# Kernel tuning notes

Measured on AMD Instinct MI355X. Metric: run time of the kernel, lower is better.

## Reference

```python
import jax, jax.numpy as jnp
import numpy as np

# --- static config (matches init_kwargs) ---
B = 2; HI = 60; WI = 60; T = 4; WS = 8; SHIFT = 4
C = 256; NH = 8; HD = C // NH; HID = 1024
P = HI * WI; N = T * P
PAD = (WS - HI % WS) % WS           # 4 -> pad 60 -> 64
HP = HI + PAD; WP = WI + PAD
NWH = HP // WS; NWW = WP // WS
L = WS * WS                          # 64 tokens per window
SCALE = HD ** -0.5

# relative position index [L, L] (constant)
_c = np.stack(np.meshgrid(np.arange(WS), np.arange(WS), indexing='ij')).reshape(2, -1)
_r = (_c[:, :, None] - _c[:, None, :]).transpose(1, 2, 0) + WS - 1
REL_IDX = jnp.asarray(_r[..., 0] * (2 * WS - 1) + _r[..., 1])

# per-window key padding mask [nWin, L] (True = padded token)
_b = np.zeros((HP, WP), bool); _b[HI:, :] = True; _b[:, WI:] = True
WIN_MASK = jnp.asarray(_b.reshape(NWH, WS, NWW, WS).transpose(0, 2, 1, 3).reshape(NWH * NWW, L))


def _ln(x, w, b):
    m = x.mean(-1, keepdims=True)
    v = jnp.square(x - m).mean(-1, keepdims=True)
    return (x - m) * jax.lax.rsqrt(v + 1e-5) * w + b


def _partition(x4):  # [Bm, HP, WP, C] -> [Bm*nWin, L, C]
    Bm = x4.shape[0]
    return x4.reshape(Bm, NWH, WS, NWW, WS, C).transpose(0, 1, 3, 2, 4, 5).reshape(Bm * NWH * NWW, L, C)


def _win_attn(xq, xkv, qw, qb, kw, kb, vw, vb, ow, ob, bias_table):
    Bm = B * T
    q4 = xq.reshape(Bm, HI, WI, C)
    k4 = xkv.reshape(Bm, HI, WI, C)
    q4 = jnp.roll(q4, (-SHIFT, -SHIFT), (1, 2))
    k4 = jnp.roll(k4, (-SHIFT, -SHIFT), (1, 2))
    pad = ((0, 0), (0, PAD), (0, PAD), (0, 0))
    q4 = jnp.pad(q4, pad); k4 = jnp.pad(k4, pad)
    q_win = _partition(q4)   # [Bw, L, C]
    kv_win = _partition(k4)
    q = (q_win @ qw.T + qb).reshape(-1, L, NH, HD)
    k = (kv_win @ kw.T + kb).reshape(-1, L, NH, HD)
    v = (kv_win @ vw.T + vb).reshape(-1, L, NH, HD)
    attn = jnp.einsum('bihd,bjhd->bhij', q, k) * SCALE
    attn = attn + bias_table[REL_IDX].transpose(2, 0, 1)[None]      # RPB [1,H,L,L]
    km = jnp.tile(WIN_MASK, (Bm, 1))                                  # [Bw, L]
    attn = jnp.where(km[:, None, None, :], -jnp.inf, attn)
    p = jax.nn.softmax(attn, axis=-1)
    o = jnp.einsum('bhij,bjhd->bihd', p, v).reshape(-1, L, C)
    o = o @ ow.T + ob
    y = o.reshape(Bm, NWH, NWW, WS, WS, C).transpose(0, 1, 3, 2, 4, 5).reshape(Bm, HP, WP, C)
    y = y[:, :HI, :WI, :]
    y = jnp.roll(y, (SHIFT, SHIFT), (1, 2))
    return y.reshape(B, N, C)


def reference(x, context, ln1_w, ln1_b, ln2_w, ln2_b, ln3_w, ln3_b, lnc_w, lnc_b,
              sa_q_w, sa_q_b, sa_k_w, sa_k_b, sa_v_w, sa_v_b, sa_o_w, sa_o_b, sa_bias,
              ca_q_w, ca_q_b, ca_k_w, ca_k_b, ca_v_w, ca_v_b, ca_o_w, ca_o_b, ca_bias,
              gamma1, gamma2, gamma_mlp, mlp_w1, mlp_b1, mlp_w2, mlp_b2):
    xn = _ln(x, ln1_w, ln1_b)
    y_s = _win_attn(xn, xn, sa_q_w, sa_q_b, sa_k_w, sa_k_b, sa_v_w, sa_v_b, sa_o_w, sa_o_b, sa_bias)
    x = x + gamma1 * y_s
    y_c = _win_attn(_ln(x, ln2_w, ln2_b), _ln(context, lnc_w, lnc_b),
                    ca_q_w, ca_q_b, ca_k_w, ca_k_b, ca_v_w, ca_v_b, ca_o_w, ca_o_b, ca_bias)
    x = x + gamma2 * y_c
    h = _ln(x, ln3_w, ln3_b)
    h = jax.nn.gelu(h @ mlp_w1.T + mlp_b1, approximate=False) @ mlp_w2.T + mlp_b2
    return x + gamma_mlp * h


def setup_inputs() -> dict:
    key = jax.random.key(0)
    ks = jax.random.split(key, 16)
    def w(k, shape, s=0.02):
        return jax.random.normal(k, shape, jnp.float32) * s
    inp = {}
    inp['x'] = jax.random.normal(ks[0], (B, N, C), jnp.float32)
    inp['context'] = jax.random.normal(ks[1], (B, N, C), jnp.float32)
    for nm in ['ln1', 'ln2', 'ln3', 'lnc']:
        inp[f'{nm}_w'] = jnp.ones((C,), jnp.float32)
        inp[f'{nm}_b'] = jnp.zeros((C,), jnp.float32)
    i = 2
    for pfx in ['sa', 'ca']:
        for pn in ['q', 'k', 'v', 'o']:
            inp[f'{pfx}_{pn}_w'] = w(ks[i], (C, C)); i += 1
            inp[f'{pfx}_{pn}_b'] = jnp.zeros((C,), jnp.float32)
        inp[f'{pfx}_bias'] = w(ks[i], ((2 * WS - 1) * (2 * WS - 1), NH)); i += 1
    inp['gamma1'] = jnp.ones((1,), jnp.float32)
    inp['gamma2'] = jnp.ones((1,), jnp.float32)
    inp['gamma_mlp'] = jnp.full((1,), 0.1, jnp.float32)
    inp['mlp_w1'] = w(ks[i], (HID, C)); i += 1
    inp['mlp_b1'] = jnp.zeros((HID,), jnp.float32)
    inp['mlp_w2'] = w(ks[i], (C, HID)); i += 1
    inp['mlp_b2'] = jnp.zeros((C,), jnp.float32)
    return inp
```

## Files before the change

kernel.cpp:

```cpp
#include <hip/hip_runtime.h>
#include <math.h>

#define BN    28800
#define CC    256
#define HIDN  1024
#define WINS  512
#define WROWS (WINS*64)
#define ATT_SCALE 0.1767766952966369f

typedef __bf16 bf16x8 __attribute__((ext_vector_type(8)));
typedef float  f32x4  __attribute__((ext_vector_type(4)));

__device__ __forceinline__ unsigned short f2bf(float f) {
    unsigned u = __float_as_uint(f);
    unsigned r = (u + 0x7FFFu + ((u >> 16) & 1u)) >> 16;
    return (unsigned short)r;
}
__device__ __forceinline__ float bf2f(unsigned short u) {
    return __uint_as_float((unsigned)u << 16);
}

__device__ __forceinline__ float gelu_f(float x) {
    float x3 = x * x * x;
    float e  = __expf(1.5957691216057308f * (x + 0.044715f * x3));
    float th = 1.0f - 2.0f * __builtin_amdgcn_rcpf(e + 1.0f);
    return 0.5f * x * (1.0f + th);
}

__device__ __forceinline__ void gl_lds16(const void* g, void* l) {
    __builtin_amdgcn_global_load_lds(
        (const __attribute__((address_space(1))) void*)g,
        (__attribute__((address_space(3))) void*)l, 16, 0, 0);
}

__global__ void ln_gather2(const float* __restrict__ x,   const float* __restrict__ w1,
                           const float* __restrict__ b1,  unsigned short* __restrict__ d1,
                           const float* __restrict__ ctx, const float* __restrict__ wc,
                           const float* __restrict__ bc,  unsigned short* __restrict__ d2) {
    const int half = blockIdx.x >> 13;
    const float* src = half ? ctx : x;
    const float* w   = half ? wc  : w1;
    const float* b   = half ? bc  : b1;
    unsigned short* dst = half ? d2 : d1;
    int row  = (int)((((blockIdx.x & 8191) * blockDim.x) + threadIdx.x) >> 6);
    int lane = threadIdx.x & 63;
    if (row >= WROWS) return;
    int win = row >> 6, l = row & 63;
    int f   = win >> 6;
    int wih = (win >> 3) & 7, wiw = win & 7;
    int r = l >> 3, s = l & 7;
    int h = wih * 8 + r, wc2 = wiw * 8 + s;
    if (h >= 60 || wc2 >= 60) {
        ushort4 z = {0, 0, 0, 0};
        reinterpret_cast<ushort4*>(dst + (size_t)row * CC)[lane] = z;
        return;
    }
    int oh = (h + 4) % 60, ow = (wc2 + 4) % 60;
    size_t tok = (size_t)f * 3600 + (size_t)oh * 60 + ow;
    float4 v = reinterpret_cast<const float4*>(src + tok * CC)[lane];
    float sm  = v.x + v.y + v.z + v.w;
    float s2 = v.x*v.x + v.y*v.y + v.z*v.z + v.w*v.w;
#pragma unroll
    for (int off = 32; off >= 1; off >>= 1) {
        sm += __shfl_xor(sm, off);
        s2 += __shfl_xor(s2, off);
    }
    float mean = sm * (1.0f / CC);
    float var  = s2 * (1.0f / CC) - mean * mean;
    float rs   = rsqrtf(var + 1e-5f);
    float4 wv = reinterpret_cast<const float4*>(w)[lane];
    float4 bv = reinterpret_cast<const float4*>(b)[lane];
    ushort4 o;
    o.x = f2bf((v.x - mean) * rs * wv.x + bv.x);
    o.y = f2bf((v.y - mean) * rs * wv.y + bv.y);
    o.z = f2bf((v.z - mean) * rs * wv.z + bv.z);
    o.w = f2bf((v.w - mean) * rs * wv.w + bv.w);
    reinterpret_cast<ushort4*>(dst + (size_t)row * CC)[lane] = o;
}

template <bool GELU, int FUSE, int TN>
__global__ __launch_bounds__(512, 4) void gemm_wa(
        const unsigned short* __restrict__ Wt,
        const unsigned short* __restrict__ a0c,
        const unsigned short* __restrict__ a1c,
        const unsigned short* __restrict__ a2c,
        const float* __restrict__ b0, const float* __restrict__ b1,
        const float* __restrict__ b2, const float* __restrict__ b3,
        unsigned short* __restrict__ o0, unsigned short* __restrict__ o1,
        unsigned short* __restrict__ o2, unsigned short* __restrict__ o3,
        int strideO, int vseg, int K, int Ntok,
        const float* __restrict__ xres, const float* __restrict__ gammap,
        float* __restrict__ fout) {
    constexpr int NW   = TN / 64;
    constexpr int BP   = TN / 128;
    constexpr int BUFB = 8192 + TN * 64;
    constexpr int POOLB = (3 * BUFB > TN * 256) ? 3 * BUFB : TN * 256;
    __shared__ __align__(16) char pool[POOLB];
    unsigned short* Cs = (unsigned short*)pool;

    const int t = threadIdx.x;
    const int w = t >> 6;
    const int l = t & 63;
    const int Mb = gridDim.x;
    int lin = blockIdx.y * Mb + blockIdx.x;
    int T = Mb * gridDim.y;
    int q = T >> 3, rr = T & 7;
    int xcd = lin & 7, slot = lin >> 3;
    int wid = (xcd < rr) ? (xcd * (q + 1) + slot)
                         : (rr * (q + 1) + (xcd - rr) * q + slot);
    const int m0 = (wid % Mb) * 128;
    const int n0 = (wid / Mb) * TN;

    const int seg = m0 >> 8;
    const unsigned short* Act = (seg == 0) ? a0c : (seg == 1) ? a1c : a2c;

    const int wr = w >> 2, wc = w & 3;
    const int r = l & 15, g = l >> 4;
    const int gp = (g ^ ((r >> 1) & 3)) * 8;
    const int srow = t >> 2;
    const int sgl  = (t & 3) ^ ((srow >> 1) & 3);

    f32x4 acc[4][NW];
#pragma unroll
    for (int i = 0; i < 4; ++i)
#pragma unroll
        for (int j = 0; j < NW; ++j) { acc[i][j][0]=0.f; acc[i][j][1]=0.f; acc[i][j][2]=0.f; acc[i][j][3]=0.f; }

#define STAGE(k0, buf)                                                             \
    do {                                                                           \
        gl_lds16(Wt + (size_t)(m0 + srow) * K + (k0) + sgl * 8,                    \
                 pool + (buf) * BUFB + w * 1024);                                  \
        _Pragma("unroll")                                                          \
        for (int p = 0; p < BP; ++p) {                                             \
            int c    = p * 512 + t;                                                \
            int rowb = c >> 2;                                                     \
            int glb  = (c & 3) ^ ((rowb >> 1) & 3);                                \
            gl_lds16(Act + (size_t)(n0 + rowb) * K + (k0) + glb * 8,               \
                     pool + (buf) * BUFB + 8192 + p * 8192 + w * 1024);            \
        }                                                                          \
    } while (0)

    STAGE(0, 0);
    STAGE(32, 1);
    const char* cb0 = pool;
    const char* cb1 = pool + BUFB;
    const char* cb2 = pool + 2 * BUFB;
    int sbuf = 2;
    const int nt = K >> 5;
    for (int kt = 0; kt < nt; ++kt) {
        if (kt < nt - 1) {
            if (TN == 128) asm volatile("s_waitcnt vmcnt(2)" ::: "memory");
            else           asm volatile("s_waitcnt vmcnt(3)" ::: "memory");
        } else {
            asm volatile("s_waitcnt vmcnt(0)" ::: "memory");
        }
        __builtin_amdgcn_s_barrier();
        __builtin_amdgcn_sched_barrier(0);
        const unsigned short* cA = (const unsigned short*)cb0;
        const unsigned short* cB = (const unsigned short*)(cb0 + 8192);
        bf16x8 bw[NW];
#pragma unroll
        for (int n = 0; n < NW; ++n)
            bw[n] = *reinterpret_cast<const bf16x8*>(&cB[(wc * (NW * 16) + n * 16 + r) * 32 + gp]);
        __builtin_amdgcn_s_setprio(1);
#pragma unroll
        for (int m = 0; m < 4; ++m) {
            bf16x8 af = *reinterpret_cast<const bf16x8*>(&cA[(wr * 64 + m * 16 + r) * 32 + gp]);
#pragma unroll
            for (int n = 0; n < NW; ++n)
                acc[m][n] = __builtin_amdgcn_mfma_f32_16x16x32_bf16(af, bw[n], acc[m][n], 0, 0, 0);
        }
        __builtin_amdgcn_s_setprio(0);
        if (kt + 2 < nt) {
            STAGE((kt + 2) * 32, sbuf);
            sbuf = (sbuf == 2) ? 0 : sbuf + 1;
        }
        const char* tmp = cb0; cb0 = cb1; cb1 = cb2; cb2 = tmp;
    }
#undef STAGE

    const float* bp = (seg == 0) ? b0 : (seg == 1) ? b1 : (seg == 2) ? b2 : b3;
    unsigned short* op = (seg == 0) ? o0 : (seg == 1) ? o1 : (seg == 2) ? o2 : o3;
    const int chseg = m0 & 255;

    if (FUSE == 0 && seg == vseg) {
#pragma unroll
        for (int m = 0; m < 4; ++m) {
            const int ch0 = chseg + wr * 64 + m * 16 + g * 4;
            float4 b4 = *reinterpret_cast<const float4*>(bp + ch0);
            const float bb[4] = {b4.x, b4.y, b4.z, b4.w};
#pragma unroll
            for (int n = 0; n < NW; ++n) {
                const int tok = n0 + wc * (NW * 16) + n * 16 + r;
#pragma unroll
                for (int j = 0; j < 4; ++j)
                    op[(size_t)(ch0 + j) * 32768 + tok] = f2bf(acc[m][n][j] + bb[j]);
            }
        }
        return;
    }

    __syncthreads();
#pragma unroll
    for (int m = 0; m < 4; ++m) {
        const int ch0 = wr * 64 + m * 16 + g * 4;
        float4 b4 = *reinterpret_cast<const float4*>(bp + chseg + ch0);
        const float bb[4] = {b4.x, b4.y, b4.z, b4.w};
#pragma unroll
        for (int n = 0; n < NW; ++n) {
            const int tok_l = wc * (NW * 16) + n * 16 + r;
            float cv[4];
#pragma unroll
            for (int j = 0; j < 4; ++j) {
                cv[j] = acc[m][n][j] + bb[j];
                if (GELU) cv[j] = gelu_f(cv[j]);
            }
            ushort4 pk;
            pk.x = f2bf(cv[0]); pk.y = f2bf(cv[1]); pk.z = f2bf(cv[2]); pk.w = f2bf(cv[3]);
            int gran = (ch0 >> 2) ^ ((tok_l & 15) << 1);
            reinterpret_cast<ushort4*>(Cs)[tok_l * 32 + gran] = pk;
        }
    }
    __syncthreads();
    const int u = t & 15, trow = t >> 4;
    if (FUSE == 0) {
#pragma unroll
        for (int it = 0; it < TN / 32; ++it) {
            int tok_l = it * 32 + trow;
            if (n0 + tok_l >= Ntok) continue;
            int up = u ^ (tok_l & 15);
            uint4 v = reinterpret_cast<const uint4*>(Cs)[tok_l * 16 + up];
            *reinterpret_cast<uint4*>(op + (size_t)(n0 + tok_l) * strideO + chseg + u * 8) = v;
        }
    } else {
        const float gsc = gammap[0];
#pragma unroll
        for (int it = 0; it < TN / 32; ++it) {
            int tok_l = it * 32 + trow;
            int wrow = n0 + tok_l;
            if (wrow >= Ntok) continue;
            int tok = wrow;
            int up = u ^ (tok_l & 15);
            uint4 v = reinterpret_cast<const uint4*>(Cs)[tok_l * 16 + up];
            const unsigned short* pu = (const unsigned short*)&v;
            const float* xr = xres + (size_t)tok * CC + chseg + u * 8;
            float4 xa = *reinterpret_cast<const float4*>(xr);
            float4 xb = *reinterpret_cast<const float4*>(xr + 4);
            float4 oa, ob;
            oa.x = xa.x + gsc * bf2f(pu[0]);
            oa.y = xa.y + gsc * bf2f(pu[1]);
            oa.z = xa.z + gsc * bf2f(pu[2]);
            oa.w = xa.w + gsc * bf2f(pu[3]);
            ob.x = xb.x + gsc * bf2f(pu[4]);
            ob.y = xb.y + gsc * bf2f(pu[5]);
            ob.z = xb.z + gsc * bf2f(pu[6]);
            ob.w = xb.w + gsc * bf2f(pu[7]);
            float* fo = fout + (size_t)tok * CC + chseg + u * 8;
            *reinterpret_cast<float4*>(fo) = oa;
            *reinterpret_cast<float4*>(fo + 4) = ob;
        }
    }
}

template <int LNM>
__global__ __launch_bounds__(512, 4) void gemm_ln(
        const unsigned short* __restrict__ Wt,
        const unsigned short* __restrict__ Act,
        const float* __restrict__ bias,
        const float* __restrict__ xres, const float* __restrict__ gammap,
        float* __restrict__ fout,
        const float* __restrict__ lnw, const float* __restrict__ lnb,
        unsigned short* __restrict__ lnout) {
    constexpr int BUFB = 16384 + 8192;
    __shared__ __align__(16) char pool[3 * BUFB];
    unsigned short* Cs = (unsigned short*)pool;

    const int t = threadIdx.x, w = t >> 6, l = t & 63;
    int lin = blockIdx.x;
    int T = gridDim.x;
    int q = T >> 3, rr = T & 7;
    int xcd = lin & 7, slot = lin >> 3;
    int wid = (xcd < rr) ? (xcd * (q + 1) + slot)
                         : (rr * (q + 1) + (xcd - rr) * q + slot);
    const int n0 = wid * 128;

    const int wr = w >> 2, wc = w & 3;
    const int r = l & 15, g = l >> 4;
    const int gp = (g ^ ((r >> 1) & 3)) * 8;
    const int K = 256;

    f32x4 acc[8][2];
#pragma unroll
    for (int i = 0; i < 8; ++i)
#pragma unroll
        for (int j = 0; j < 2; ++j) { acc[i][j][0]=0.f; acc[i][j][1]=0.f; acc[i][j][2]=0.f; acc[i][j][3]=0.f; }

#define STAGE(k0, buf)                                                             \
    do {                                                                           \
        _Pragma("unroll")                                                          \
        for (int p = 0; p < 2; ++p) {                                              \
            int c    = p * 512 + t;                                                \
            int rowa = c >> 2;                                                     \
            int gla  = (c & 3) ^ ((rowa >> 1) & 3);                                \
            gl_lds16(Wt + (size_t)rowa * K + (k0) + gla * 8,                       \
                     pool + (buf) * BUFB + (p * 512 + w * 64) * 16);               \
        }                                                                          \
        {                                                                          \
            int rowb = t >> 2;                                                     \
            int glb  = (t & 3) ^ ((rowb >> 1) & 3);                                \
            gl_lds16(Act + (size_t)(n0 + rowb) * K + (k0) + glb * 8,               \
                     pool + (buf) * BUFB + 16384 + w * 1024);                      \
        }                                                                          \
    } while (0)

    STAGE(0, 0);
    STAGE(32, 1);
    const char* cb0 = pool;
    const char* cb1 = pool + BUFB;
    const char* cb2 = pool + 2 * BUFB;
    int sbuf = 2;
    for (int kt = 0; kt < 8; ++kt) {
        if (kt < 7) asm volatile("s_waitcnt vmcnt(3)" ::: "memory");
        else        asm volatile("s_waitcnt vmcnt(0)" ::: "memory");
        __builtin_amdgcn_s_barrier();
        __builtin_amdgcn_sched_barrier(0);
        const unsigned short* cA = (const unsigned short*)cb0;
        const unsigned short* cB = (const unsigned short*)(cb0 + 16384);
        bf16x8 bw[2];
#pragma unroll
        for (int n = 0; n < 2; ++n)
            bw[n] = *reinterpret_cast<const bf16x8*>(&cB[(wc * 32 + n * 16 + r) * 32 + gp]);
        __builtin_amdgcn_s_setprio(1);
#pragma unroll
        for (int m = 0; m < 8; ++m) {
            bf16x8 af = *reinterpret_cast<const bf16x8*>(&cA[(wr * 128 + m * 16 + r) * 32 + gp]);
#pragma unroll
            for (int n = 0; n < 2; ++n)
                acc[m][n] = __builtin_amdgcn_mfma_f32_16x16x32_bf16(af, bw[n], acc[m][n], 0, 0, 0);
        }
        __builtin_amdgcn_s_setprio(0);
        if (kt + 2 < 8) {
            STAGE((kt + 2) * 32, sbuf);
            sbuf = (sbuf == 2) ? 0 : sbuf + 1;
        }
        const char* tmp = cb0; cb0 = cb1; cb1 = cb2; cb2 = tmp;
    }
#undef STAGE

    __syncthreads();
#pragma unroll
    for (int m = 0; m < 8; ++m) {
        const int ch0 = wr * 128 + m * 16 + g * 4;
        float4 b4 = *reinterpret_cast<const float4*>(bias + ch0);
        const float bb[4] = {b4.x, b4.y, b4.z, b4.w};
#pragma unroll
        for (int n = 0; n < 2; ++n) {
            const int tokh = wc * 32 + n * 16 + r;
            ushort4 pk;
            pk.x = f2bf(acc[m][n][0] + bb[0]);
            pk.y = f2bf(acc[m][n][1] + bb[1]);
            pk.z = f2bf(acc[m][n][2] + bb[2]);
            pk.w = f2bf(acc[m][n][3] + bb[3]);
            int gran = (ch0 >> 2) ^ ((tokh & 15) << 1);
            reinterpret_cast<ushort4*>(Cs)[tokh * 64 + gran] = pk;
        }
    }
    __syncthreads();

    const float gsc = gammap[0];
    const int u16 = t & 31, trow = t >> 5;
#pragma unroll
    for (int it = 0; it < 8; ++it) {
        int rowh = it * 16 + trow;
        int wrow = n0 + rowh;
        int win = wrow >> 6, l2 = wrow & 63;
        int f = win >> 6, wih = (win >> 3) & 7, wiw = win & 7;
        int r2 = l2 >> 3, s2 = l2 & 7;
        int hh = wih * 8 + r2, wcol = wiw * 8 + s2;
        bool pad = (hh >= 60) || (wcol >= 60);
        if (pad) {
            if (LNM == 1) {
                uint4 z = {0u, 0u, 0u, 0u};
                *reinterpret_cast<uint4*>(lnout + (size_t)wrow * CC + u16 * 8) = z;
            }
            continue;
        }
        int oh = hh + 4; if (oh >= 60) oh -= 60;
        int ow = wcol + 4; if (ow >= 60) ow -= 60;
        int tok = f * 3600 + oh * 60 + ow;

        int up = u16 ^ (rowh & 15);
        uint4 v = reinterpret_cast<const uint4*>(Cs)[rowh * 32 + up];
        const unsigned short* pu = (const unsigned short*)&v;
        const float* xr = xres + (size_t)tok * CC + u16 * 8;
        float4 xa = *reinterpret_cast<const float4*>(xr);
        float4 xb = *reinterpret_cast<const float4*>(xr + 4);
        float4 oa, ob;
        oa.x = xa.x + gsc * bf2f(pu[0]);
        oa.y = xa.y + gsc * bf2f(pu[1]);
        oa.z = xa.z + gsc * bf2f(pu[2]);
        oa.w = xa.w + gsc * bf2f(pu[3]);
        ob.x = xb.x + gsc * bf2f(pu[4]);
        ob.y = xb.y + gsc * bf2f(pu[5]);
        ob.z = xb.z + gsc * bf2f(pu[6]);
        ob.w = xb.w + gsc * bf2f(pu[7]);
        float* fo = fout + (size_t)tok * CC + u16 * 8;
        *reinterpret_cast<float4*>(fo) = oa;
        *reinterpret_cast<float4*>(fo + 4) = ob;

        float sm = oa.x + oa.y + oa.z + oa.w + ob.x + ob.y + ob.z + ob.w;
        float s2q = oa.x*oa.x + oa.y*oa.y + oa.z*oa.z + oa.w*oa.w
                  + ob.x*ob.x + ob.y*ob.y + ob.z*ob.z + ob.w*ob.w;
#pragma unroll
        for (int off = 1; off <= 16; off <<= 1) {
            sm  += __shfl_xor(sm, off);
            s2q += __shfl_xor(s2q, off);
        }
        float mean = sm * (1.0f / CC);
        float rs   = rsqrtf(s2q * (1.0f / CC) - mean * mean + 1e-5f);
        float4 w0 = *reinterpret_cast<const float4*>(lnw + u16 * 8);
        float4 w1 = *reinterpret_cast<const float4*>(lnw + u16 * 8 + 4);
        float4 c0 = *reinterpret_cast<const float4*>(lnb + u16 * 8);
        float4 c1 = *reinterpret_cast<const float4*>(lnb + u16 * 8 + 4);
        ushort4 pa, pb;
        pa.x = f2bf((oa.x - mean) * rs * w0.x + c0.x);
        pa.y = f2bf((oa.y - mean) * rs * w0.y + c0.y);
        pa.z = f2bf((oa.z - mean) * rs * w0.z + c0.z);
        pa.w = f2bf((oa.w - mean) * rs * w0.w + c0.w);
        pb.x = f2bf((ob.x - mean) * rs * w1.x + c1.x);
        pb.y = f2bf((ob.y - mean) * rs * w1.y + c1.y);
        pb.z = f2bf((ob.z - mean) * rs * w1.z + c1.z);
        pb.w = f2bf((ob.w - mean) * rs * w1.w + c1.w);
        size_t dst = (size_t)((LNM == 1) ? wrow : tok) * CC + u16 * 8;
        *reinterpret_cast<ushort4*>(lnout + dst)     = pa;
        *reinterpret_cast<ushort4*>(lnout + dst + 4) = pb;
    }
}

__global__ __launch_bounds__(256) void attn_mfma(
        const unsigned short* __restrict__ Q,
        const unsigned short* __restrict__ K,
        const unsigned short* __restrict__ VT,
        const float* __restrict__ biasx,
        unsigned short* __restrict__ AO) {
    __shared__ __align__(16) unsigned short Pl[4][64 * 64];
    const int t = threadIdx.x;
    const int w = t >> 6, l = t & 63;
    const int win = blockIdx.x >> 1;
    const int h   = (blockIdx.x & 1) * 4 + w;
    const int c = l & 15, g = l >> 4;
    const int wih = (win >> 3) & 7, wiw = win & 7;
    const size_t qkbase = (size_t)win * 64 * CC + (size_t)h * 32;

    bf16x8 ka[4], qb[4];
#pragma unroll
    for (int mj = 0; mj < 4; ++mj)
        ka[mj] = *reinterpret_cast<const bf16x8*>(K + qkbase + (size_t)(mj * 16 + c) * CC + g * 8);
#pragma unroll
    for (int ni = 0; ni < 4; ++ni)
        qb[ni] = *reinterpret_cast<const bf16x8*>(Q + qkbase + (size_t)(ni * 16 + c) * CC + g * 8);
    f32x4 s[4][4];
#pragma unroll
    for (int mj = 0; mj < 4; ++mj)
#pragma unroll
        for (int ni = 0; ni < 4; ++ni) { s[mj][ni][0]=0.f; s[mj][ni][1]=0.f; s[mj][ni][2]=0.f; s[mj][ni][3]=0.f; }
#pragma unroll
    for (int mj = 0; mj < 4; ++mj)
#pragma unroll
        for (int ni = 0; ni < 4; ++ni)
            s[mj][ni] = __builtin_amdgcn_mfma_f32_16x16x32_bf16(ka[mj], qb[ni], s[mj][ni], 0, 0, 0);

    const float* bx = biasx + h * 4096;
    const bool modd = (wiw == 7) && (g & 1);
#pragma unroll
    for (int mj = 0; mj < 4; ++mj) {
        const bool mmj = (wih == 7) && (mj >= 2);
#pragma unroll
        for (int ni = 0; ni < 4; ++ni) {
            float4 b4 = *reinterpret_cast<const float4*>(bx + (ni * 16 + c) * 64 + mj * 16 + g * 4);
            const float bb[4] = {b4.x, b4.y, b4.z, b4.w};
#pragma unroll
            for (int jj = 0; jj < 4; ++jj) {
                float v = s[mj][ni][jj] * ATT_SCALE + bb[jj];
                s[mj][ni][jj] = (mmj || modd) ? -1e30f : v;
            }
        }
    }

#pragma unroll
    for (int ni = 0; ni < 4; ++ni) {
        float mx = -1e30f;
#pragma unroll
        for (int mj = 0; mj < 4; ++mj)
#pragma unroll
            for (int jj = 0; jj < 4; ++jj) mx = fmaxf(mx, s[mj][ni][jj]);
        mx = fmaxf(mx, __shfl_xor(mx, 16));
        mx = fmaxf(mx, __shfl_xor(mx, 32));
        float sum = 0.f;
#pragma unroll
        for (int mj = 0; mj < 4; ++mj)
#pragma unroll
            for (int jj = 0; jj < 4; ++jj) {
                float p = __expf(s[mj][ni][jj] - mx);
                s[mj][ni][jj] = p;
                sum += p;
            }
        sum += __shfl_xor(sum, 16);
        sum += __shfl_xor(sum, 32);
        float rinv = __builtin_amdgcn_rcpf(sum);
        const int i  = ni * 16 + c;
        const int ik = i & 7;
#pragma unroll
        for (int mj = 0; mj < 4; ++mj) {
            ushort4 pk;
            pk.x = f2bf(s[mj][ni][0] * rinv);
            pk.y = f2bf(s[mj][ni][1] * rinv);
            pk.z = f2bf(s[mj][ni][2] * rinv);
            pk.w = f2bf(s[mj][ni][3] * rinv);
            int chunk = (mj * 2 + (g >> 1)) ^ ik;
            *reinterpret_cast<ushort4*>((char*)&Pl[w][0] + i * 128 + chunk * 16 + (g & 1) * 8) = pk;
        }
    }

    bf16x8 vb[2][2];
#pragma unroll
    for (int nd = 0; nd < 2; ++nd)
#pragma unroll
        for (int kt = 0; kt < 2; ++kt)
            vb[nd][kt] = *reinterpret_cast<const bf16x8*>(
                VT + (size_t)(h * 32 + nd * 16 + c) * 32768 + win * 64 + kt * 32 + g * 8);
    f32x4 o[4][2];
#pragma unroll
    for (int mi = 0; mi < 4; ++mi)
#pragma unroll
        for (int nd = 0; nd < 2; ++nd) { o[mi][nd][0]=0.f; o[mi][nd][1]=0.f; o[mi][nd][2]=0.f; o[mi][nd][3]=0.f; }
#pragma unroll
    for (int mi = 0; mi < 4; ++mi) {
        const int i  = mi * 16 + c;
        const int ik = i & 7;
#pragma unroll
        for (int kt = 0; kt < 2; ++kt) {
            int chunk = (kt * 4 + g) ^ ik;
            bf16x8 pa = *reinterpret_cast<const bf16x8*>((char*)&Pl[w][0] + i * 128 + chunk * 16);
#pragma unroll
            for (int nd = 0; nd < 2; ++nd)
                o[mi][nd] = __builtin_amdgcn_mfma_f32_16x16x32_bf16(pa, vb[nd][kt], o[mi][nd], 0, 0, 0);
        }
    }

    unsigned short* AOs = &Pl[0][0];
    __syncthreads();
#pragma unroll
    for (int mi = 0; mi < 4; ++mi)
#pragma unroll
        for (int nd = 0; nd < 2; ++nd)
#pragma unroll
            for (int jj = 0; jj < 4; ++jj)
                AOs[(mi * 16 + g * 4 + jj) * 136 + w * 32 + nd * 16 + c] = f2bf(o[mi][nd][jj]);
    __syncthreads();
    unsigned short* aop = AO + (size_t)win * 64 * CC + (blockIdx.x & 1) * 128;
    const int u = t & 15, rr2 = t >> 4;
#pragma unroll
    for (int it = 0; it < 4; ++it) {
        int row = it * 16 + rr2;
        uint4 v = *reinterpret_cast<const uint4*>(&AOs[row * 136 + u * 8]);
        *reinterpret_cast<uint4*>(aop + (size_t)row * CC + u * 8) = v;
    }
}

__global__ void cvt_bias(const float* s0, const float* s1, const float* s2, const float* s3,
                         const float* s4, const float* s5, const float* s6, const float* s7,
                         const float* s8, const float* s9, unsigned short* __restrict__ dst,
                         const float* __restrict__ sa, const float* __restrict__ ca,
                         float* __restrict__ biasx) {
    int blk = blockIdx.x;
    if (blk >= 1024) {
        int e = (blk - 1024) * 256 + threadIdx.x;
        const float* src = (e < 16384) ? sa : ca;
        int e2 = e & 16383;
        int h = e2 >> 12, ij = e2 & 4095, i = ij >> 6, j = ij & 63;
        int ri = i >> 3, si = i & 7, rj = j >> 3, sj = j & 7;
        biasx[e] = src[((ri - rj + 7) * 15 + (si - sj + 7)) * 8 + h];
        return;
    }
    const float* srcs[10] = {s0, s1, s2, s3, s4, s5, s6, s7, s8, s9};
    int wi = (blk < 512) ? (blk >> 6) : (blk < 768 ? 8 : 9);
    size_t start = (wi < 8) ? (size_t)wi * 65536 : (wi == 8 ? (size_t)524288 : (size_t)786432);
    size_t gidx = (size_t)blk * 1024 + (size_t)threadIdx.x * 4;
    float4 v = *reinterpret_cast<const float4*>(srcs[wi] + (gidx - start));
    ushort4 o;
    o.x = f2bf(v.x); o.y = f2bf(v.y); o.z = f2bf(v.z); o.w = f2bf(v.w);
    *reinterpret_cast<ushort4*>(dst + gidx) = o;
}

extern "C" void kernel_launch(void* const* d_in, const int* in_sizes, int n_in,
                              void* d_out, int out_size, void* d_ws, size_t ws_size,
                              hipStream_t stream) {
    const float* x    = (const float*)d_in[0];
    const float* ctx  = (const float*)d_in[1];
    const float* ln1w = (const float*)d_in[2];
    const float* ln1b = (const float*)d_in[3];
    const float* ln2w = (const float*)d_in[4];
    const float* ln2b = (const float*)d_in[5];
    const float* ln3w = (const float*)d_in[6];
    const float* ln3b = (const float*)d_in[7];
    const float* lncw = (const float*)d_in[8];
    const float* lncb = (const float*)d_in[9];
    const float* saqw = (const float*)d_in[10];
    const float* saqb = (const float*)d_in[11];
    const float* sakw = (const float*)d_in[12];
    const float* sakb = (const float*)d_in[13];
    const float* savw = (const float*)d_in[14];
    const float* savb = (const float*)d_in[15];
    const float* saow = (const float*)d_in[16];
    const float* saob = (const float*)d_in[17];
    const float* sabias = (const float*)d_in[18];
    const float* caqw = (const float*)d_in[19];
    const float* caqb = (const float*)d_in[20];
    const float* cakw = (const float*)d_in[21];
    const float* cakb = (const float*)d_in[22];
    const float* cavw = (const float*)d_in[23];
    const float* cavb = (const float*)d_in[24];
    const float* caow = (const float*)d_in[25];
    const float* caob = (const float*)d_in[26];
    const float* cabias = (const float*)d_in[27];
    const float* gamma1 = (const float*)d_in[28];
    const float* gamma2 = (const float*)d_in[29];
    const float* gammam = (const float*)d_in[30];
    const float* mw1 = (const float*)d_in[31];
    const float* mb1 = (const float*)d_in[32];
    const float* mw2 = (const float*)d_in[33];
    const float* mb2 = (const float*)d_in[34];

    float* ws = (float*)d_ws;
    unsigned short* LNbf = (unsigned short*)(ws);
    unsigned short* Gq   = (unsigned short*)(ws + 3686400);
    unsigned short* Gkv  = (unsigned short*)(ws + 7880704);
    unsigned short* Qbf  = (unsigned short*)(ws + 12075008);
    unsigned short* Kbf  = (unsigned short*)(ws + 16269312);
    unsigned short* VTbf = (unsigned short*)(ws + 20463616);
    unsigned short* AObf = (unsigned short*)(ws + 24657920);
    float* X1  = ws + 28852224;
    unsigned short* Wp = (unsigned short*)(ws + 36225024);
    float* biasx = ws + 36749312;
    unsigned short* H1bf = Qbf;

    unsigned short* w_saqkv = Wp;
    unsigned short* w_sao   = Wp + 196608;
    unsigned short* w_caqkv = Wp + 262144;
    unsigned short* w_cao   = Wp + 458752;
    unsigned short* w_m1    = Wp + 524288;
    unsigned short* w_m2    = Wp + 786432;

    float* OUT = (float*)d_out;

    dim3 blk(256);
    dim3 blk512(512);
    dim3 gAttn(WINS * 2);

    cvt_bias<<<dim3(1152), blk, 0, stream>>>(saqw, sakw, savw, saow, caqw, cakw, cavw, caow,
                                             mw1, mw2, Wp, sabias, cabias, biasx);
    ln_gather2<<<dim3(16384), blk, 0, stream>>>(x, ln1w, ln1b, Gq, ctx, lncw, lncb, Gkv);

    gemm_wa<false,0,256><<<dim3(6, 128), blk512, 0, stream>>>(w_saqkv, Gq, Gq, Gq,
                                                              saqb, sakb, savb, savb,
                                                              Qbf, Kbf, VTbf, VTbf, CC, 2, CC, WROWS,
                                                              nullptr, nullptr, nullptr);
    attn_mfma<<<gAttn, blk, 0, stream>>>(Qbf, Kbf, VTbf, biasx, AObf);
    gemm_ln<1><<<dim3(256), blk512, 0, stream>>>(w_sao, AObf, saob, x, gamma1, X1, ln2w, ln2b, Gq);

    gemm_wa<false,0,256><<<dim3(6, 128), blk512, 0, stream>>>(w_caqkv, Gq, Gkv, Gkv,
                                                              caqb, cakb, cavb, cavb,
                                                              Qbf, Kbf, VTbf, VTbf, CC, 2, CC, WROWS,
                                                              nullptr, nullptr, nullptr);
    attn_mfma<<<gAttn, blk, 0, stream>>>(Qbf, Kbf, VTbf, biasx + 16384, AObf);
    gemm_ln<2><<<dim3(256), blk512, 0, stream>>>(w_cao, AObf, caob, X1, gamma2, X1, ln3w, ln3b, LNbf);

    gemm_wa<true,0,256><<<dim3(8, 113), blk512, 0, stream>>>(w_m1, LNbf, LNbf, LNbf,
                                                             mb1, mb1 + 256, mb1 + 512, mb1 + 768,
                                                             H1bf, H1bf + 256, H1bf + 512, H1bf + 768,
                                                             HIDN, -1, CC, BN, nullptr, nullptr, nullptr);
    gemm_wa<false,2,128><<<dim3(2, 225), blk512, 0, stream>>>(w_m2, H1bf, H1bf, H1bf,
                                                             mb2, mb2, mb2, mb2,
                                                             Qbf, Qbf, Qbf, Qbf, CC, -1, HIDN, BN,
                                                             X1, gammam, OUT);
}
```

Before: 213.8 us.

## Add dedicated 256-thread GEMM kernel for MLP first layer with GELU

Replaces the generic 512-thread gemm_wa launch for the MLP up-projection with a new gemm_big kernel. It uses 256 threads, each wave computing a larger 128x64 register tile (8x4 MFMA accumulators), a triple-buffered LDS pipeline with async global-to-LDS loads, and XCD-aware block remapping. The fused bias+GELU epilogue is written through swizzled LDS. The goal is higher per-wave data reuse and better latency hiding, at the cost of more registers per thread and potentially lower occupancy.

```diff
diff --git a/kernel.cpp b/kernel.cpp
--- a/kernel.cpp
+++ b/kernel.cpp
@@ -259,6 +259,127 @@
             *reinterpret_cast<float4*>(fo) = oa;
             *reinterpret_cast<float4*>(fo + 4) = ob;
         }
+    }
+}
+
+template <bool GELU>
+__global__ __launch_bounds__(256, 2) void gemm_big(
+        const unsigned short* __restrict__ Wt,
+        const unsigned short* __restrict__ Act,
+        const float* __restrict__ bias,
+        unsigned short* __restrict__ out,
+        int strideO, int K, int Ntok) {
+    constexpr int BUFB = 8192 + 16384;
+    __shared__ __align__(16) char pool[3 * BUFB];
+    unsigned short* Cs = (unsigned short*)pool;
+
+    const int t = threadIdx.x;
+    const int w = t >> 6;
+    const int l = t & 63;
+    const int Mb = gridDim.x;
+    int lin = blockIdx.y * Mb + blockIdx.x;
+    int T = Mb * gridDim.y;
+    int q = T >> 3, rr = T & 7;
+    int xcd = lin & 7, slot = lin >> 3;
+    int wid = (xcd < rr) ? (xcd * (q + 1) + slot)
+                         : (rr * (q + 1) + (xcd - rr) * q + slot);
+    const int m0 = (wid % Mb) * 128;
+    const int n0 = (wid / Mb) * 256;
+
+    const int r = l & 15, g = l >> 4;
+    const int gp = (g ^ ((r >> 1) & 3)) * 8;
+
+    f32x4 acc[8][4];
+#pragma unroll
+    for (int i = 0; i < 8; ++i)
+#pragma unroll
+        for (int j = 0; j < 4; ++j) { acc[i][j][0]=0.f; acc[i][j][1]=0.f; acc[i][j][2]=0.f; acc[i][j][3]=0.f; }
+
+#define STAGEB(k0, buf)                                                            \
+    do {                                                                           \
+        _Pragma("unroll")                                                          \
+        for (int p = 0; p < 2; ++p) {                                              \
+            int c    = p * 256 + t;                                                \
+            int rowa = c >> 2;                                                     \
+            int gla  = (c & 3) ^ ((rowa >> 1) & 3);                                \
+            gl_lds16(Wt + (size_t)(m0 + rowa) * K + (k0) + gla * 8,                \
+                     pool + (buf) * BUFB + (p * 256 + w * 64) * 16);               \
+        }                                                                          \
+        _Pragma("unroll")                                                          \
+        for (int p = 0; p < 4; ++p) {                                              \
+            int c    = p * 256 + t;                                                \
+            int rowb = c >> 2;                                                     \
+            int glb  = (c & 3) ^ ((rowb >> 1) & 3);                                \
+            gl_lds16(Act + (size_t)(n0 + rowb) * K + (k0) + glb * 8,               \
+                     pool + (buf) * BUFB + 8192 + (p * 256 + w * 64) * 16);        \
+        }                                                                          \
+    } while (0)
+
+    STAGEB(0, 0);
+    STAGEB(32, 1);
+    const char* cb0 = pool;
+    const char* cb1 = pool + BUFB;
+    const char* cb2 = pool + 2 * BUFB;
+    int sbuf = 2;
+    const int nt = K >> 5;
+    for (int kt = 0; kt < nt; ++kt) {
+        if (kt < nt - 1) asm volatile("s_waitcnt vmcnt(6)" ::: "memory");
+        else             asm volatile("s_waitcnt vmcnt(0)" ::: "memory");
+        __builtin_amdgcn_s_barrier();
+        __builtin_amdgcn_sched_barrier(0);
+        const unsigned short* cA = (const unsigned short*)cb0;
+        const unsigned short* cB = (const unsigned short*)(cb0 + 8192);
+        bf16x8 bw[4];
+#pragma unroll
+        for (int n = 0; n < 4; ++n)
+            bw[n] = *reinterpret_cast<const bf16x8*>(&cB[(w * 64 + n * 16 + r) * 32 + gp]);
+        __builtin_amdgcn_s_setprio(1);
+#pragma unroll
+        for (int m = 0; m < 8; ++m) {
+            bf16x8 af = *reinterpret_cast<const bf16x8*>(&cA[(m * 16 + r) * 32 + gp]);
+#pragma unroll
+            for (int n = 0; n < 4; ++n)
+                acc[m][n] = __builtin_amdgcn_mfma_f32_16x16x32_bf16(af, bw[n], acc[m][n], 0, 0, 0);
+        }
+        __builtin_amdgcn_s_setprio(0);
+        if (kt + 2 < nt) {
+            STAGEB((kt + 2) * 32, sbuf);
+            sbuf = (sbuf == 2) ? 0 : sbuf + 1;
+        }
+        const char* tmp = cb0; cb0 = cb1; cb1 = cb2; cb2 = tmp;
+    }
+#undef STAGEB
+
+    __syncthreads();
+#pragma unroll
+    for (int m = 0; m < 8; ++m) {
+        const int ch0 = m * 16 + g * 4;
+        float4 b4 = *reinterpret_cast<const float4*>(bias + m0 + ch0);
+        const float bb[4] = {b4.x, b4.y, b4.z, b4.w};
+#pragma unroll
+        for (int n = 0; n < 4; ++n) {
+            const int tok_l = w * 64 + n * 16 + r;
+            float cv[4];
+#pragma unroll
+            for (int j = 0; j < 4; ++j) {
+                cv[j] = acc[m][n][j] + bb[j];
+                if (GELU) cv[j] = gelu_f(cv[j]);
+            }
+            ushort4 pk;
+            pk.x = f2bf(cv[0]); pk.y = f2bf(cv[1]); pk.z = f2bf(cv[2]); pk.w = f2bf(cv[3]);
+            int gran = (ch0 >> 2) ^ ((tok_l & 15) << 1);
+            reinterpret_cast<ushort4*>(Cs)[tok_l * 32 + gran] = pk;
+        }
+    }
+    __syncthreads();
+    const int u = t & 15, trow = t >> 4;
+#pragma unroll
+    for (int it = 0; it < 16; ++it) {
+        int tok_l = it * 16 + trow;
+        if (n0 + tok_l >= Ntok) continue;
+        int up = u ^ (tok_l & 15);
+        uint4 v = reinterpret_cast<const uint4*>(Cs)[tok_l * 16 + up];
+        *reinterpret_cast<uint4*>(out + (size_t)(n0 + tok_l) * strideO + m0 + u * 8) = v;
     }
 }
 
@@ -676,10 +797,7 @@
     attn_mfma<<<gAttn, blk, 0, stream>>>(Qbf, Kbf, VTbf, biasx + 16384, AObf);
     gemm_ln<2><<<dim3(256), blk512, 0, stream>>>(w_cao, AObf, caob, X1, gamma2, X1, ln3w, ln3b, LNbf);
 
-    gemm_wa<true,0,256><<<dim3(8, 113), blk512, 0, stream>>>(w_m1, LNbf, LNbf, LNbf,
-                                                             mb1, mb1 + 256, mb1 + 512, mb1 + 768,
-                                                             H1bf, H1bf + 256, H1bf + 512, H1bf + 768,
-                                                             HIDN, -1, CC, BN, nullptr, nullptr, nullptr);
+    gemm_big<true><<<dim3(8, 113), blk, 0, stream>>>(w_m1, LNbf, mb1, H1bf, HIDN, CC, BN);
     gemm_wa<false,2,128><<<dim3(2, 225), blk512, 0, stream>>>(w_m2, H1bf, H1bf, H1bf,
                                                              mb2, mb2, mb2, mb2,
                                                              Qbf, Qbf, Qbf, Qbf, CC, -1, HIDN, BN,
```

New measurement: 214.8 us. Within noise of the previous version (+0.5%).
